# Performance work log

Hardware: AMD Instinct MI355X
Metric: run time of the kernel (lower is better)

The kernel has to match this reference:

```python
import jax, jax.numpy as jnp
import numpy as np

T, H, E, I = 1024, 1024, 64, 512          # tokens, hidden, n_routed_experts, moe_intermediate
NG, TKG, TOPK = 8, 3, 6                   # n_group, topk_group, num_experts_per_tok
NSH = 2                                   # n_shared_experts
RSF = 2.5                                 # routed_scaling_factor
SI = NSH * I                              # shared-expert intermediate


def setup_inputs() -> dict:
    key = jax.random.key(0)
    ks = jax.random.split(key, 9)
    s = 0.02
    return {
        "hidden_states": jax.random.normal(ks[0], (T, H), jnp.float32),
        "gate_w": jax.random.normal(ks[1], (H, E), jnp.float32) * s,
        "e_bias": jax.random.normal(ks[2], (E,), jnp.float32) * s,
        "w_gate": jax.random.normal(ks[3], (E, H, I), jnp.float32) * s,
        "w_up": jax.random.normal(ks[4], (E, H, I), jnp.float32) * s,
        "w_down": jax.random.normal(ks[5], (E, I, H), jnp.float32) * s,
        "sw_gate": jax.random.normal(ks[6], (H, SI), jnp.float32) * s,
        "sw_up": jax.random.normal(ks[7], (H, SI), jnp.float32) * s,
        "sw_down": jax.random.normal(ks[8], (SI, H), jnp.float32) * s,
    }


def _silu_mlp(x, wg, wu, wd):
    # DeepseekV2MLP: down( silu(gate(x)) * up(x) )
    return (jax.nn.silu(x @ wg) * (x @ wu)) @ wd


def _grouped_topk(logits, e_bias):
    # noaux_tc: sigmoid scoring; bias only influences selection, not weights
    scores = jax.nn.sigmoid(logits)                       # [T, E]
    sc = scores + e_bias
    # group score = sum of top-2 biased scores within each group
    gsc = jax.lax.top_k(sc.reshape(-1, NG, E // NG), 2)[0].sum(-1)   # [T, NG]
    gidx = jax.lax.top_k(gsc, TKG)[1]                     # [T, TKG]
    rows = jnp.arange(sc.shape[0])[:, None]
    gmask = jnp.zeros_like(gsc).at[rows, gidx].set(1.0)   # [T, NG]
    emask = jnp.repeat(gmask, E // NG, axis=1) > 0        # [T, E]
    masked = jnp.where(emask, sc, -jnp.inf)
    topk_ids = jax.lax.top_k(masked, TOPK)[1]             # [T, TOPK]
    w = jnp.take_along_axis(scores, topk_ids, axis=1)     # unbiased scores
    w = w / w.sum(-1, keepdims=True)                      # renormalize (norm_topk_prob)
    return w, topk_ids


def reference(hidden_states, gate_w, e_bias, w_gate, w_up, w_down, sw_gate, sw_up, sw_down):
    x = hidden_states
    logits = x @ gate_w                                   # [T, E]
    w, ids = _grouped_topk(logits, e_bias)
    rows = jnp.arange(x.shape[0])[:, None]
    dense_w = jnp.zeros((x.shape[0], E), x.dtype).at[rows, ids].set(w)  # [T, E]

    def body(acc, ws):
        wg, wu, wd, we = ws                               # we: [T] combine weights for this expert
        return acc + we[:, None] * _silu_mlp(x, wg, wu, wd), None

    routed, _ = jax.lax.scan(body, jnp.zeros_like(x), (w_gate, w_up, w_down, dense_w.T))
    shared = _silu_mlp(x, sw_gate, sw_up, sw_down)
    return routed * RSF + shared
```

## Files before the change

kernel.cpp:

```cpp
#include <hip/hip_runtime.h>
#include <hip/hip_bf16.h>

#define T_TOK 1024
#define HDIM  1024
#define NEXP  64
#define IDIM  512
#define SIDIM 1024
#define NGRP  8
#define GSZ   8
#define TKGN  3
#define TOPKN 6
#define CAPS  14336

typedef __attribute__((ext_vector_type(8))) short bf16x8;
typedef __attribute__((ext_vector_type(4))) float f32x4;

__device__ __forceinline__ short f2bf(float f) {
  union { __hip_bfloat16 h; short s; } u;
  u.h = __float2bfloat16(f);
  return u.s;
}
__device__ __forceinline__ float bf2f(short s) {
  union { float f; unsigned u; } c;
  c.u = ((unsigned)(unsigned short)s) << 16;
  return c.f;
}

#define BARRIER() asm volatile("s_waitcnt lgkmcnt(0)\n\ts_barrier" ::: "memory")

__global__ void k0_init(int* counts, int* cursor) {
  int i = threadIdx.x;
  if (i < NEXP) { counts[i] = 0; cursor[i] = 0; }
}

__global__ __launch_bounds__(256) void k1_gate(
    const float* __restrict__ x, const float* __restrict__ gw,
    const float* __restrict__ ebias,
    int* __restrict__ ids, float* __restrict__ wts, int* __restrict__ counts) {
  int sub = threadIdx.x >> 6;
  int lane = threadIdx.x & 63;
  int t = blockIdx.x * 4 + sub;
  const float* xr = x + (size_t)t * HDIM;
  double a0 = 0.0, a1 = 0.0, a2 = 0.0, a3 = 0.0;
  for (int h = 0; h < HDIM; h += 4) {
    float4 xv = *(const float4*)(xr + h);
    a0 += (double)xv.x * (double)gw[(h + 0) * NEXP + lane];
    a1 += (double)xv.y * (double)gw[(h + 1) * NEXP + lane];
    a2 += (double)xv.z * (double)gw[(h + 2) * NEXP + lane];
    a3 += (double)xv.w * (double)gw[(h + 3) * NEXP + lane];
  }
  float logit = (float)((a0 + a1) + (a2 + a3));
  float sig = 1.f / (1.f + expf(-logit));
  float sc = sig + ebias[lane];
  __shared__ float s_sc[4][NEXP], s_sig[4][NEXP];
  s_sc[sub][lane] = sc; s_sig[sub][lane] = sig;
  __syncthreads();
  if (lane == 0) {
    const float* ssc = s_sc[sub];
    const float* ssig = s_sig[sub];
    float gsum[NGRP];
    for (int g = 0; g < NGRP; ++g) {
      float m1 = -1e30f; int i1 = -1;
      for (int i = 0; i < GSZ; ++i) {
        float v = ssc[g * GSZ + i];
        if (v > m1) { m1 = v; i1 = i; }
      }
      float m2 = -1e30f;
      for (int i = 0; i < GSZ; ++i) {
        if (i == i1) continue;
        float v = ssc[g * GSZ + i];
        if (v > m2) m2 = v;
      }
      gsum[g] = m1 + m2;
    }
    unsigned gselmask = 0;
    for (int r = 0; r < TKGN; ++r) {
      float best = -1e30f; int bi = 0;
      for (int g = 0; g < NGRP; ++g) {
        if ((gselmask >> g) & 1) continue;
        if (gsum[g] > best) { best = gsum[g]; bi = g; }
      }
      gselmask |= 1u << bi;
    }
    unsigned long long taken = 0;
    int chosen[TOPKN]; float wsum = 0.f;
    for (int r = 0; r < TOPKN; ++r) {
      float best = -1e30f; int bi = 0;
      for (int e = 0; e < NEXP; ++e) {
        if (!((gselmask >> (e >> 3)) & 1)) continue;
        if ((taken >> e) & 1) continue;
        float v = ssc[e];
        if (v > best) { best = v; bi = e; }
      }
      taken |= 1ull << bi;
      chosen[r] = bi;
      wsum += ssig[bi];
    }
    for (int r = 0; r < TOPKN; ++r) {
      ids[t * TOPKN + r] = chosen[r];
      wts[t * TOPKN + r] = ssig[chosen[r]] / wsum;
      atomicAdd(&counts[chosen[r]], 1);
    }
  }
}

__global__ void k1b_scan(const int* __restrict__ counts, int* __restrict__ eoff,
                         int* __restrict__ tile_e, int* __restrict__ tile_base,
                         int* __restrict__ nt_p, int* __restrict__ slot_tok) {
  __shared__ int soff[NEXP + 1];
  __shared__ int s_total;
  int tid = threadIdx.x;
  if (tid == 0) {
    int o = 0, idx = 0;
    for (int e = 0; e < NEXP; ++e) {
      soff[e] = o;
      int ntile = (counts[e] + 127) >> 7;
      for (int t2 = 0; t2 < ntile; ++t2) { tile_e[idx] = e; tile_base[idx] = o + t2 * 128; ++idx; }
      o += ntile << 7;
    }
    soff[NEXP] = o; nt_p[0] = idx; s_total = o;
  }
  __syncthreads();
  if (tid <= NEXP) eoff[tid] = soff[tid];
  int total = s_total;
  for (int i = tid; i < total; i += blockDim.x) slot_tok[i] = 0;
}

__global__ void k1c_fill(const int* __restrict__ ids,
                         const int* __restrict__ eoff, int* __restrict__ cursor,
                         int* __restrict__ slot_tok, int* __restrict__ tslot) {
  int i = blockIdx.x * blockDim.x + threadIdx.x;
  if (i >= T_TOK * TOPKN) return;
  int e = ids[i];
  int s = eoff[e] + atomicAdd(&cursor[e], 1);
  slot_tok[s] = i / TOPKN;
  tslot[i] = s;
}

__device__ __forceinline__ void tile_mid(
    const float* __restrict__ x, const float* __restrict__ wg, const float* __restrict__ wu,
    const int* __restrict__ slot_tok, int rowbase, int ic0, int IC,
    __hip_bfloat16* __restrict__ mid, short* As, short* Bg, short* Bu) {
  int tid = threadIdx.x;
  int wave = tid >> 6, lane = tid & 63;
  int wm = wave >> 1, wn = wave & 1;
  int lr = lane & 15, lk = lane >> 4;

  int ar = tid >> 3, kg = tid & 7;
  int aw0 = (ar * 8 + (kg ^ (ar & 7))) * 8;
  int aw1 = ((ar + 64) * 8 + (kg ^ (ar & 7))) * 8;
  int tok0 = slot_tok ? slot_tok[rowbase + ar] : (rowbase + ar);
  int tok1 = slot_tok ? slot_tok[rowbase + ar + 64] : (rowbase + ar + 64);
  const float* aptr0 = x + (size_t)tok0 * HDIM + kg * 8;
  const float* aptr1 = x + (size_t)tok1 * HDIM + kg * 8;

  int bn = tid & 63, bkg = tid >> 6;
  const float* bgp = wg + (size_t)(bkg * 8) * IC + ic0 + bn;
  const float* bup = wu + (size_t)(bkg * 8) * IC + ic0 + bn;
  int bw = (bn * 8 + (bkg ^ (bn & 7))) * 8;

  f32x4 accg[2][2], accu[2][2];
  #pragma unroll
  for (int a = 0; a < 2; ++a)
    #pragma unroll
    for (int b = 0; b < 2; ++b) { accg[a][b] = (f32x4)0.f; accu[a][b] = (f32x4)0.f; }

  float4 a00, a01, a10, a11;
  float bgr[8], bur[8];

  auto LOAD = [&](int s) {
    const float* p0 = aptr0 + s * 64;
    const float* p1 = aptr1 + s * 64;
    a00 = *(const float4*)p0; a01 = *(const float4*)(p0 + 4);
    a10 = *(const float4*)p1; a11 = *(const float4*)(p1 + 4);
    #pragma unroll
    for (int i = 0; i < 8; ++i) {
      bgr[i] = bgp[(size_t)(s * 64 + i) * IC];
      bur[i] = bup[(size_t)(s * 64 + i) * IC];
    }
  };
  auto STORE = [&](int b) {
    short* as = As + b * 8192;
    short* bg = Bg + b * 4096;
    short* bu = Bu + b * 4096;
    bf16x8 t0, t1;
    t0[0] = f2bf(a00.x); t0[1] = f2bf(a00.y); t0[2] = f2bf(a00.z); t0[3] = f2bf(a00.w);
    t0[4] = f2bf(a01.x); t0[5] = f2bf(a01.y); t0[6] = f2bf(a01.z); t0[7] = f2bf(a01.w);
    t1[0] = f2bf(a10.x); t1[1] = f2bf(a10.y); t1[2] = f2bf(a10.z); t1[3] = f2bf(a10.w);
    t1[4] = f2bf(a11.x); t1[5] = f2bf(a11.y); t1[6] = f2bf(a11.z); t1[7] = f2bf(a11.w);
    *(bf16x8*)&as[aw0] = t0;
    *(bf16x8*)&as[aw1] = t1;
    bf16x8 tg, tu;
    #pragma unroll
    for (int i = 0; i < 8; ++i) { tg[i] = f2bf(bgr[i]); tu[i] = f2bf(bur[i]); }
    *(bf16x8*)&bg[bw] = tg;
    *(bf16x8*)&bu[bw] = tu;
  };
  auto COMPUTE = [&](int b) {
    const short* as = As + b * 8192;
    const short* bg = Bg + b * 4096;
    const short* bu = Bu + b * 4096;
    #pragma unroll
    for (int kk = 0; kk < 2; ++kk) {
      bf16x8 af[2];
      #pragma unroll
      for (int mf = 0; mf < 2; ++mf) {
        int row = wm * 32 + mf * 16 + lr;
        af[mf] = *(const bf16x8*)&as[(row * 8 + ((kk * 4 + lk) ^ (row & 7))) * 8];
      }
      #pragma unroll
      for (int nf = 0; nf < 2; ++nf) {
        int col = wn * 32 + nf * 16 + lr;
        int gi = (col * 8 + ((kk * 4 + lk) ^ (col & 7))) * 8;
        bf16x8 bgf = *(const bf16x8*)&bg[gi];
        bf16x8 buf_ = *(const bf16x8*)&bu[gi];
        #pragma unroll
        for (int mf = 0; mf < 2; ++mf) {
          accg[mf][nf] = __builtin_amdgcn_mfma_f32_16x16x32_bf16(af[mf], bgf, accg[mf][nf], 0, 0, 0);
          accu[mf][nf] = __builtin_amdgcn_mfma_f32_16x16x32_bf16(af[mf], buf_, accu[mf][nf], 0, 0, 0);
        }
      }
    }
  };

  const int NST = HDIM / 64;
  LOAD(0);
  STORE(0);
  LOAD(1);
  BARRIER();
  for (int s = 0; s < NST; ++s) {
    COMPUTE(s & 1);
    if (s + 1 < NST) {
      STORE((s + 1) & 1);
      if (s + 2 < NST) LOAD(s + 2);
      BARRIER();
    }
  }

  #pragma unroll
  for (int mf = 0; mf < 2; ++mf)
    #pragma unroll
    for (int nf = 0; nf < 2; ++nf)
      #pragma unroll
      for (int r = 0; r < 4; ++r) {
        int row = wm * 32 + mf * 16 + lk * 4 + r;
        int col = wn * 32 + nf * 16 + lr;
        float gv = accg[mf][nf][r], uv = accu[mf][nf][r];
        float h = gv / (1.f + expf(-gv)) * uv;
        mid[(size_t)(rowbase + row) * IC + ic0 + col] = __float2bfloat16(h);
      }
}

__device__ __forceinline__ void tile_down(
    const __hip_bfloat16* __restrict__ mid, const float* __restrict__ wd,
    int rowbase, int n0, int KD,
    __hip_bfloat16* __restrict__ dout, short* As, short* Bs) {
  int tid = threadIdx.x;
  int wave = tid >> 6, lane = tid & 63;
  int wm = wave >> 1, wn = wave & 1;
  int lr = lane & 15, lk = lane >> 4;

  int ar = tid >> 3, kg = tid & 7;
  int aw0 = (ar * 8 + (kg ^ (ar & 7))) * 8;
  int aw1 = ((ar + 64) * 8 + (kg ^ (ar & 7))) * 8;
  const __hip_bfloat16* aptr0 = mid + (size_t)(rowbase + ar) * KD + kg * 8;
  const __hip_bfloat16* aptr1 = mid + (size_t)(rowbase + ar + 64) * KD + kg * 8;

  int bn = tid & 63, bkg = tid >> 6;
  const float* bp = wd + (size_t)(bkg * 8) * HDIM + n0 + bn;
  int bw = (bn * 8 + (bkg ^ (bn & 7))) * 8;

  f32x4 acc[2][2];
  #pragma unroll
  for (int a = 0; a < 2; ++a)
    #pragma unroll
    for (int b = 0; b < 2; ++b) acc[a][b] = (f32x4)0.f;

  bf16x8 av0, av1;
  float br[8];

  auto LOAD = [&](int s) {
    av0 = *(const bf16x8*)(aptr0 + s * 64);
    av1 = *(const bf16x8*)(aptr1 + s * 64);
    #pragma unroll
    for (int i = 0; i < 8; ++i) br[i] = bp[(size_t)(s * 64 + i) * HDIM];
  };
  auto STORE = [&](int b) {
    short* as = As + b * 8192;
    short* bs = Bs + b * 4096;
    *(bf16x8*)&as[aw0] = av0;
    *(bf16x8*)&as[aw1] = av1;
    bf16x8 tb;
    #pragma unroll
    for (int i = 0; i < 8; ++i) tb[i] = f2bf(br[i]);
    *(bf16x8*)&bs[bw] = tb;
  };
  auto COMPUTE = [&](int b) {
    const short* as = As + b * 8192;
    const short* bs = Bs + b * 4096;
    #pragma unroll
    for (int kk = 0; kk < 2; ++kk) {
      bf16x8 af[2];
      #pragma unroll
      for (int mf = 0; mf < 2; ++mf) {
        int row = wm * 32 + mf * 16 + lr;
        af[mf] = *(const bf16x8*)&as[(row * 8 + ((kk * 4 + lk) ^ (row & 7))) * 8];
      }
      #pragma unroll
      for (int nf = 0; nf < 2; ++nf) {
        int col = wn * 32 + nf * 16 + lr;
        bf16x8 bf_ = *(const bf16x8*)&bs[(col * 8 + ((kk * 4 + lk) ^ (col & 7))) * 8];
        #pragma unroll
        for (int mf = 0; mf < 2; ++mf)
          acc[mf][nf] = __builtin_amdgcn_mfma_f32_16x16x32_bf16(af[mf], bf_, acc[mf][nf], 0, 0, 0);
      }
    }
  };

  const int NST = KD / 64;
  LOAD(0);
  STORE(0);
  LOAD(1);
  BARRIER();
  for (int s = 0; s < NST; ++s) {
    COMPUTE(s & 1);
    if (s + 1 < NST) {
      STORE((s + 1) & 1);
      if (s + 2 < NST) LOAD(s + 2);
      BARRIER();
    }
  }

  #pragma unroll
  for (int mf = 0; mf < 2; ++mf)
    #pragma unroll
    for (int nf = 0; nf < 2; ++nf)
      #pragma unroll
      for (int r = 0; r < 4; ++r) {
        int row = wm * 32 + mf * 16 + lk * 4 + r;
        int col = wn * 32 + nf * 16 + lr;
        dout[(size_t)(rowbase + row) * HDIM + n0 + col] = __float2bfloat16(acc[mf][nf][r]);
      }
}

__global__ __launch_bounds__(512) void k2_fused(
    const float* __restrict__ x, const float* __restrict__ Wg, const float* __restrict__ Wu,
    const float* __restrict__ swg, const float* __restrict__ swu,
    const int* __restrict__ slot_tok, const int* __restrict__ tile_e,
    const int* __restrict__ tile_base, const int* __restrict__ nt_p,
    __hip_bfloat16* __restrict__ mid_r, __hip_bfloat16* __restrict__ mid_s) {
  __shared__ __align__(16) short As[2 * 8192];
  __shared__ __align__(16) short Bg[2 * 4096];
  __shared__ __align__(16) short Bu[2 * 4096];
  int nrt = nt_p[0] * 8;
  int nitems = nrt + 128;
  for (int item = blockIdx.x; item < nitems; item += gridDim.x) {
    if (item < nrt) {
      int tile = item >> 3, c = item & 7;
      int e = tile_e[tile];
      tile_mid(x, Wg + (size_t)e * HDIM * IDIM, Wu + (size_t)e * HDIM * IDIM,
               slot_tok, tile_base[tile], c * 64, IDIM, mid_r, As, Bg, Bu);
    } else {
      int it = item - nrt;
      int mt = it >> 4, c = it & 15;
      tile_mid(x, swg, swu, nullptr, mt * 128, c * 64, SIDIM, mid_s, As, Bg, Bu);
    }
  }
}

__global__ __launch_bounds__(512) void k3_fused(
    const __hip_bfloat16* __restrict__ mid_r, const __hip_bfloat16* __restrict__ mid_s,
    const float* __restrict__ Wd, const float* __restrict__ swd,
    const int* __restrict__ tile_e, const int* __restrict__ tile_base,
    const int* __restrict__ nt_p,
    __hip_bfloat16* __restrict__ dout_r, __hip_bfloat16* __restrict__ dout_s) {
  __shared__ __align__(16) short As[2 * 8192];
  __shared__ __align__(16) short Bs[2 * 4096];
  int nrt = nt_p[0] * 16;
  int nsh = 128;
  int nitems = nrt + nsh;
  for (int item = blockIdx.x; item < nitems; item += gridDim.x) {
    if (item < nsh) {
      int mt = item >> 4, c = item & 15;
      tile_down(mid_s, swd, mt * 128, c * 64, SIDIM, dout_s, As, Bs);
    } else {
      int it = item - nsh;
      int tile = it >> 4, c = it & 15;
      int e = tile_e[tile];
      tile_down(mid_r, Wd + (size_t)e * IDIM * HDIM, tile_base[tile], c * 64, IDIM,
                dout_r, As, Bs);
    }
  }
}

__global__ __launch_bounds__(128) void k4_combine(
    const __hip_bfloat16* __restrict__ dout_r, const __hip_bfloat16* __restrict__ dout_s,
    const int* __restrict__ tslot, const float* __restrict__ wts,
    float* __restrict__ out) {
  int t = blockIdx.x;
  int tid = threadIdx.x;
  int sl[TOPKN]; float w[TOPKN];
  #pragma unroll
  for (int r = 0; r < TOPKN; ++r) {
    sl[r] = tslot[t * TOPKN + r];
    w[r] = wts[t * TOPKN + r] * 2.5f;
  }
  int h0 = tid * 8;
  float acc[8];
  bf16x8 vs = *(const bf16x8*)((const short*)dout_s + (size_t)t * HDIM + h0);
  #pragma unroll
  for (int j = 0; j < 8; ++j) acc[j] = bf2f(vs[j]);
  #pragma unroll
  for (int r = 0; r < TOPKN; ++r) {
    bf16x8 v = *(const bf16x8*)((const short*)dout_r + (size_t)sl[r] * HDIM + h0);
    #pragma unroll
    for (int j = 0; j < 8; ++j) acc[j] += w[r] * bf2f(v[j]);
  }
  float* op = out + (size_t)t * HDIM + h0;
  float4 o0 = make_float4(acc[0], acc[1], acc[2], acc[3]);
  float4 o1 = make_float4(acc[4], acc[5], acc[6], acc[7]);
  *(float4*)op = o0;
  *(float4*)(op + 4) = o1;
}

extern "C" void kernel_launch(void* const* d_in, const int* in_sizes, int n_in,
                              void* d_out, int out_size, void* d_ws, size_t ws_size,
                              hipStream_t stream) {
  (void)in_sizes; (void)n_in; (void)out_size; (void)ws_size;
  const float* x      = (const float*)d_in[0];
  const float* gate_w = (const float*)d_in[1];
  const float* ebias  = (const float*)d_in[2];
  const float* wgate  = (const float*)d_in[3];
  const float* wup    = (const float*)d_in[4];
  const float* wdown  = (const float*)d_in[5];
  const float* swg    = (const float*)d_in[6];
  const float* swu    = (const float*)d_in[7];
  const float* swd    = (const float*)d_in[8];
  float* out = (float*)d_out;

  char* ws = (char*)d_ws;
  int*   counts    = (int*)(ws + 0);
  int*   cursor    = (int*)(ws + 256);
  int*   eoff      = (int*)(ws + 512);
  int*   nt_p      = (int*)(ws + 1024);
  int*   tile_e    = (int*)(ws + 1088);
  int*   tile_base = (int*)(ws + 1600);
  int*   ids       = (int*)(ws + 4096);
  float* wts       = (float*)(ws + 28672);
  int*   tslot     = (int*)(ws + 53248);
  int*   slot_tok  = (int*)(ws + 77824);
  __hip_bfloat16* mid_r  = (__hip_bfloat16*)(ws + 135168);
  __hip_bfloat16* mid_s  = mid_r + (size_t)CAPS * IDIM;
  __hip_bfloat16* dout_r = (__hip_bfloat16*)(ws + 16912384);
  __hip_bfloat16* dout_s = dout_r + (size_t)CAPS * HDIM;

  k0_init<<<1, 128, 0, stream>>>(counts, cursor);
  k1_gate<<<T_TOK / 4, 256, 0, stream>>>(x, gate_w, ebias, ids, wts, counts);
  k1b_scan<<<1, 256, 0, stream>>>(counts, eoff, tile_e, tile_base, nt_p, slot_tok);
  k1c_fill<<<(T_TOK * TOPKN + 255) / 256, 256, 0, stream>>>(ids, eoff, cursor, slot_tok, tslot);
  k2_fused<<<640, 512, 0, stream>>>(x, wgate, wup, swg, swu, slot_tok, tile_e, tile_base, nt_p, mid_r, mid_s);
  k3_fused<<<1152, 512, 0, stream>>>(mid_r, mid_s, wdown, swd, tile_e, tile_base, nt_p, dout_r, dout_s);
  k4_combine<<<T_TOK, 128, 0, stream>>>(dout_r, dout_s, tslot, wts, out);
}
```

Measured before the change: 232.5 us.

## Deepen weight prefetch to two stages ahead and cap occupancy in MoE GEMM kernels

Splits the A and B tile loads and keeps two register sets of weight values, so fp32 weight loads are issued two K-steps ahead instead of one, and unrolls the main loop by two with fixed LDS buffers. It also adds a min-blocks-per-SM hint of 4 to both fused GEMM kernels and changes the persistent grid sizes to 512 blocks. The aim is to hide global-memory latency on the strided weight reads. The cost is extra registers under a tighter register budget, which could cause spills.

```diff
diff --git a/kernel.cpp b/kernel.cpp
--- a/kernel.cpp
+++ b/kernel.cpp
@@ -166,20 +166,22 @@
     for (int b = 0; b < 2; ++b) { accg[a][b] = (f32x4)0.f; accu[a][b] = (f32x4)0.f; }
 
   float4 a00, a01, a10, a11;
-  float bgr[8], bur[8];
-
-  auto LOAD = [&](int s) {
+  float g0[8], u0[8], g1[8], u1[8];
+
+  auto LOADA = [&](int s) {
     const float* p0 = aptr0 + s * 64;
     const float* p1 = aptr1 + s * 64;
     a00 = *(const float4*)p0; a01 = *(const float4*)(p0 + 4);
     a10 = *(const float4*)p1; a11 = *(const float4*)(p1 + 4);
+  };
+  auto LOADB = [&](float (&g)[8], float (&u)[8], int s) {
     #pragma unroll
     for (int i = 0; i < 8; ++i) {
-      bgr[i] = bgp[(size_t)(s * 64 + i) * IC];
-      bur[i] = bup[(size_t)(s * 64 + i) * IC];
-    }
-  };
-  auto STORE = [&](int b) {
+      g[i] = bgp[(size_t)(s * 64 + i) * IC];
+      u[i] = bup[(size_t)(s * 64 + i) * IC];
+    }
+  };
+  auto STORE = [&](int b, float (&g)[8], float (&u)[8]) {
     short* as = As + b * 8192;
     short* bg = Bg + b * 4096;
     short* bu = Bu + b * 4096;
@@ -192,7 +194,7 @@
     *(bf16x8*)&as[aw1] = t1;
     bf16x8 tg, tu;
     #pragma unroll
-    for (int i = 0; i < 8; ++i) { tg[i] = f2bf(bgr[i]); tu[i] = f2bf(bur[i]); }
+    for (int i = 0; i < 8; ++i) { tg[i] = f2bf(g[i]); tu[i] = f2bf(u[i]); }
     *(bf16x8*)&bg[bw] = tg;
     *(bf16x8*)&bu[bw] = tu;
   };
@@ -224,15 +226,24 @@
   };
 
   const int NST = HDIM / 64;
-  LOAD(0);
-  STORE(0);
-  LOAD(1);
+  LOADB(g0, u0, 0);
+  LOADB(g1, u1, 1);
+  LOADA(0);
+  STORE(0, g0, u0);
+  LOADA(1);
+  LOADB(g0, u0, 2);
   BARRIER();
-  for (int s = 0; s < NST; ++s) {
-    COMPUTE(s & 1);
-    if (s + 1 < NST) {
-      STORE((s + 1) & 1);
-      if (s + 2 < NST) LOAD(s + 2);
+  for (int s = 0; s < NST; s += 2) {
+    COMPUTE(0);
+    STORE(1, g1, u1);
+    if (s + 2 < NST) LOADA(s + 2);
+    if (s + 3 < NST) LOADB(g1, u1, s + 3);
+    BARRIER();
+    COMPUTE(1);
+    if (s + 2 < NST) {
+      STORE(0, g0, u0);
+      if (s + 3 < NST) LOADA(s + 3);
+      if (s + 4 < NST) LOADB(g0, u0, s + 4);
       BARRIER();
     }
   }
@@ -277,27 +288,29 @@
     for (int b = 0; b < 2; ++b) acc[a][b] = (f32x4)0.f;
 
   bf16x8 av0, av1;
-  float br[8];
-
-  auto LOAD = [&](int s) {
+  float b0[8], b1[8];
+
+  auto LOADA = [&](int s) {
     av0 = *(const bf16x8*)(aptr0 + s * 64);
     av1 = *(const bf16x8*)(aptr1 + s * 64);
-    #pragma unroll
-    for (int i = 0; i < 8; ++i) br[i] = bp[(size_t)(s * 64 + i) * HDIM];
-  };
-  auto STORE = [&](int b) {
-    short* as = As + b * 8192;
-    short* bs = Bs + b * 4096;
+  };
+  auto LOADB = [&](float (&b)[8], int s) {
+    #pragma unroll
+    for (int i = 0; i < 8; ++i) b[i] = bp[(size_t)(s * 64 + i) * HDIM];
+  };
+  auto STORE = [&](int bb, float (&b)[8]) {
+    short* as = As + bb * 8192;
+    short* bs = Bs + bb * 4096;
     *(bf16x8*)&as[aw0] = av0;
     *(bf16x8*)&as[aw1] = av1;
     bf16x8 tb;
     #pragma unroll
-    for (int i = 0; i < 8; ++i) tb[i] = f2bf(br[i]);
+    for (int i = 0; i < 8; ++i) tb[i] = f2bf(b[i]);
     *(bf16x8*)&bs[bw] = tb;
   };
-  auto COMPUTE = [&](int b) {
-    const short* as = As + b * 8192;
-    const short* bs = Bs + b * 4096;
+  auto COMPUTE = [&](int bb) {
+    const short* as = As + bb * 8192;
+    const short* bs = Bs + bb * 4096;
     #pragma unroll
     for (int kk = 0; kk < 2; ++kk) {
       bf16x8 af[2];
@@ -318,15 +331,24 @@
   };
 
   const int NST = KD / 64;
-  LOAD(0);
-  STORE(0);
-  LOAD(1);
+  LOADB(b0, 0);
+  LOADB(b1, 1);
+  LOADA(0);
+  STORE(0, b0);
+  LOADA(1);
+  LOADB(b0, 2);
   BARRIER();
-  for (int s = 0; s < NST; ++s) {
-    COMPUTE(s & 1);
-    if (s + 1 < NST) {
-      STORE((s + 1) & 1);
-      if (s + 2 < NST) LOAD(s + 2);
+  for (int s = 0; s < NST; s += 2) {
+    COMPUTE(0);
+    STORE(1, b1);
+    if (s + 2 < NST) LOADA(s + 2);
+    if (s + 3 < NST) LOADB(b1, s + 3);
+    BARRIER();
+    COMPUTE(1);
+    if (s + 2 < NST) {
+      STORE(0, b0);
+      if (s + 3 < NST) LOADA(s + 3);
+      if (s + 4 < NST) LOADB(b0, s + 4);
       BARRIER();
     }
   }
@@ -343,7 +365,7 @@
       }
 }
 
-__global__ __launch_bounds__(512) void k2_fused(
+__global__ __launch_bounds__(512, 4) void k2_fused(
     const float* __restrict__ x, const float* __restrict__ Wg, const float* __restrict__ Wu,
     const float* __restrict__ swg, const float* __restrict__ swu,
     const int* __restrict__ slot_tok, const int* __restrict__ tile_e,
@@ -368,7 +390,7 @@
   }
 }
 
-__global__ __launch_bounds__(512) void k3_fused(
+__global__ __launch_bounds__(512, 4) void k3_fused(
     const __hip_bfloat16* __restrict__ mid_r, const __hip_bfloat16* __restrict__ mid_s,
     const float* __restrict__ Wd, const float* __restrict__ swd,
     const int* __restrict__ tile_e, const int* __restrict__ tile_base,
@@ -458,7 +480,7 @@
   k1_gate<<<T_TOK / 4, 256, 0, stream>>>(x, gate_w, ebias, ids, wts, counts);
   k1b_scan<<<1, 256, 0, stream>>>(counts, eoff, tile_e, tile_base, nt_p, slot_tok);
   k1c_fill<<<(T_TOK * TOPKN + 255) / 256, 256, 0, stream>>>(ids, eoff, cursor, slot_tok, tslot);
-  k2_fused<<<640, 512, 0, stream>>>(x, wgate, wup, swg, swu, slot_tok, tile_e, tile_base, nt_p, mid_r, mid_s);
-  k3_fused<<<1152, 512, 0, stream>>>(mid_r, mid_s, wdown, swd, tile_e, tile_base, nt_p, dout_r, dout_s);
+  k2_fused<<<512, 512, 0, stream>>>(x, wgate, wup, swg, swu, slot_tok, tile_e, tile_base, nt_p, mid_r, mid_s);
+  k3_fused<<<512, 512, 0, stream>>>(mid_r, mid_s, wdown, swd, tile_e, tile_base, nt_p, dout_r, dout_s);
   k4_combine<<<T_TOK, 128, 0, stream>>>(dout_r, dout_s, tslot, wts, out);
 }
```

Result: slower. 246.8 us (+6.2%).

## Pre-transpose weights to bf16 and stage GEMM tiles via direct global-to-LDS loads

Applied to the files above, without the earlier changes.

Adds kernels that convert x to bf16 and transpose every expert and shared weight into K-contiguous bf16 layouts each call. The GEMM tiles then stage A and B with global_load_lds 16-byte copies into swizzled LDS, replacing strided fp32 scalar loads and register conversion. The persistent grid loops become one tile per block with an XCD-aware block remap. The cost is an extra full read and write of all weights (about 200MB of fp32 input) every call, plus more kernel launches.

```diff
diff --git a/kernel.cpp b/kernel.cpp
--- a/kernel.cpp
+++ b/kernel.cpp
@@ -26,11 +26,57 @@
   return c.f;
 }
 
-#define BARRIER() asm volatile("s_waitcnt lgkmcnt(0)\n\ts_barrier" ::: "memory")
+__device__ __forceinline__ void gld16(const void* g, void* l) {
+  typedef __attribute__((address_space(1))) const unsigned int GU;
+  typedef __attribute__((address_space(3))) unsigned int LU;
+  __builtin_amdgcn_global_load_lds((GU*)g, (LU*)l, 16, 0, 0);
+}
+
+#define PIPE_BARRIER() asm volatile("s_waitcnt vmcnt(0) lgkmcnt(0)\n\ts_barrier" ::: "memory")
 
 __global__ void k0_init(int* counts, int* cursor) {
   int i = threadIdx.x;
   if (i < NEXP) { counts[i] = 0; cursor[i] = 0; }
+}
+
+__global__ __launch_bounds__(128) void kx_conv(const float* __restrict__ x,
+                                               __hip_bfloat16* __restrict__ xb) {
+  int row = blockIdx.x;
+  int c = threadIdx.x * 8;
+  const float* s = x + (size_t)row * HDIM + c;
+  float4 v0 = *(const float4*)s;
+  float4 v1 = *(const float4*)(s + 4);
+  bf16x8 o;
+  o[0] = f2bf(v0.x); o[1] = f2bf(v0.y); o[2] = f2bf(v0.z); o[3] = f2bf(v0.w);
+  o[4] = f2bf(v1.x); o[5] = f2bf(v1.y); o[6] = f2bf(v1.z); o[7] = f2bf(v1.w);
+  *(bf16x8*)((short*)xb + (size_t)row * HDIM + c) = o;
+}
+
+__global__ __launch_bounds__(256) void kt_transpose(
+    const float* __restrict__ src, __hip_bfloat16* __restrict__ dst, int R, int C) {
+  __shared__ float t[64 * 65];
+  int m = blockIdx.z;
+  const float* s = src + (size_t)m * R * C + (size_t)(blockIdx.x * 64) * C + blockIdx.y * 64;
+  short* d = (short*)dst + (size_t)m * R * C + (size_t)(blockIdx.y * 64) * R + blockIdx.x * 64;
+  int tid = threadIdx.x;
+  int r = tid >> 2, c16 = (tid & 3) * 16;
+  const float* sp = s + (size_t)r * C + c16;
+  #pragma unroll
+  for (int j = 0; j < 4; ++j) {
+    float4 v = *(const float4*)(sp + j * 4);
+    t[r * 65 + c16 + j * 4 + 0] = v.x;
+    t[r * 65 + c16 + j * 4 + 1] = v.y;
+    t[r * 65 + c16 + j * 4 + 2] = v.z;
+    t[r * 65 + c16 + j * 4 + 3] = v.w;
+  }
+  __syncthreads();
+  bf16x8 o0, o1;
+  #pragma unroll
+  for (int j = 0; j < 8; ++j) o0[j] = f2bf(t[(c16 + j) * 65 + r]);
+  #pragma unroll
+  for (int j = 0; j < 8; ++j) o1[j] = f2bf(t[(c16 + 8 + j) * 65 + r]);
+  *(bf16x8*)(d + (size_t)r * R + c16) = o0;
+  *(bf16x8*)(d + (size_t)r * R + c16 + 8) = o1;
 }
 
 __global__ __launch_bounds__(256) void k1_gate(
@@ -137,27 +183,26 @@
   tslot[i] = s;
 }
 
-__device__ __forceinline__ void tile_mid(
-    const float* __restrict__ x, const float* __restrict__ wg, const float* __restrict__ wu,
+__device__ __forceinline__ void tile_mid2(
+    const __hip_bfloat16* __restrict__ xb,
+    const __hip_bfloat16* __restrict__ wtg, const __hip_bfloat16* __restrict__ wtu,
     const int* __restrict__ slot_tok, int rowbase, int ic0, int IC,
-    __hip_bfloat16* __restrict__ mid, short* As, short* Bg, short* Bu) {
+    __hip_bfloat16* __restrict__ mid,
+    short* As, short* Bg, short* Bu) {
   int tid = threadIdx.x;
   int wave = tid >> 6, lane = tid & 63;
   int wm = wave >> 1, wn = wave & 1;
   int lr = lane & 15, lk = lane >> 4;
 
-  int ar = tid >> 3, kg = tid & 7;
-  int aw0 = (ar * 8 + (kg ^ (ar & 7))) * 8;
-  int aw1 = ((ar + 64) * 8 + (kg ^ (ar & 7))) * 8;
-  int tok0 = slot_tok ? slot_tok[rowbase + ar] : (rowbase + ar);
-  int tok1 = slot_tok ? slot_tok[rowbase + ar + 64] : (rowbase + ar + 64);
-  const float* aptr0 = x + (size_t)tok0 * HDIM + kg * 8;
-  const float* aptr1 = x + (size_t)tok1 * HDIM + kg * 8;
-
-  int bn = tid & 63, bkg = tid >> 6;
-  const float* bgp = wg + (size_t)(bkg * 8) * IC + ic0 + bn;
-  const float* bup = wu + (size_t)(bkg * 8) * IC + ic0 + bn;
-  int bw = (bn * 8 + (bkg ^ (bn & 7))) * 8;
+  int srow = wave * 8 + (lane >> 3);
+  int kgl = (lane & 7) ^ (srow & 7);
+  int t0 = slot_tok ? slot_tok[rowbase + srow] : (rowbase + srow);
+  int t1 = slot_tok ? slot_tok[rowbase + srow + 64] : (rowbase + srow + 64);
+  const short* ga0 = (const short*)xb + (size_t)t0 * HDIM + kgl * 8;
+  const short* ga1 = (const short*)xb + (size_t)t1 * HDIM + kgl * 8;
+  const short* gbg = (const short*)wtg + (size_t)(ic0 + srow) * HDIM + kgl * 8;
+  const short* gbu = (const short*)wtu + (size_t)(ic0 + srow) * HDIM + kgl * 8;
+  int ldsoff = wave * 1024;
 
   f32x4 accg[2][2], accu[2][2];
   #pragma unroll
@@ -165,53 +210,31 @@
     #pragma unroll
     for (int b = 0; b < 2; ++b) { accg[a][b] = (f32x4)0.f; accu[a][b] = (f32x4)0.f; }
 
-  float4 a00, a01, a10, a11;
-  float bgr[8], bur[8];
-
-  auto LOAD = [&](int s) {
-    const float* p0 = aptr0 + s * 64;
-    const float* p1 = aptr1 + s * 64;
-    a00 = *(const float4*)p0; a01 = *(const float4*)(p0 + 4);
-    a10 = *(const float4*)p1; a11 = *(const float4*)(p1 + 4);
-    #pragma unroll
-    for (int i = 0; i < 8; ++i) {
-      bgr[i] = bgp[(size_t)(s * 64 + i) * IC];
-      bur[i] = bup[(size_t)(s * 64 + i) * IC];
-    }
+  auto STAGE = [&](int buf, int s) {
+    char* a = (char*)As + buf * 16384 + ldsoff;
+    char* bg = (char*)Bg + buf * 8192 + ldsoff;
+    char* bu = (char*)Bu + buf * 8192 + ldsoff;
+    gld16(ga0 + s * 64, a);
+    gld16(ga1 + s * 64, a + 8192);
+    gld16(gbg + s * 64, bg);
+    gld16(gbu + s * 64, bu);
   };
-  auto STORE = [&](int b) {
-    short* as = As + b * 8192;
-    short* bg = Bg + b * 4096;
-    short* bu = Bu + b * 4096;
-    bf16x8 t0, t1;
-    t0[0] = f2bf(a00.x); t0[1] = f2bf(a00.y); t0[2] = f2bf(a00.z); t0[3] = f2bf(a00.w);
-    t0[4] = f2bf(a01.x); t0[5] = f2bf(a01.y); t0[6] = f2bf(a01.z); t0[7] = f2bf(a01.w);
-    t1[0] = f2bf(a10.x); t1[1] = f2bf(a10.y); t1[2] = f2bf(a10.z); t1[3] = f2bf(a10.w);
-    t1[4] = f2bf(a11.x); t1[5] = f2bf(a11.y); t1[6] = f2bf(a11.z); t1[7] = f2bf(a11.w);
-    *(bf16x8*)&as[aw0] = t0;
-    *(bf16x8*)&as[aw1] = t1;
-    bf16x8 tg, tu;
-    #pragma unroll
-    for (int i = 0; i < 8; ++i) { tg[i] = f2bf(bgr[i]); tu[i] = f2bf(bur[i]); }
-    *(bf16x8*)&bg[bw] = tg;
-    *(bf16x8*)&bu[bw] = tu;
-  };
-  auto COMPUTE = [&](int b) {
-    const short* as = As + b * 8192;
-    const short* bg = Bg + b * 4096;
-    const short* bu = Bu + b * 4096;
+  auto COMPUTE = [&](int buf) {
+    const short* as = As + buf * 8192;
+    const short* bg = Bg + buf * 4096;
+    const short* bu = Bu + buf * 4096;
     #pragma unroll
     for (int kk = 0; kk < 2; ++kk) {
       bf16x8 af[2];
       #pragma unroll
       for (int mf = 0; mf < 2; ++mf) {
         int row = wm * 32 + mf * 16 + lr;
-        af[mf] = *(const bf16x8*)&as[(row * 8 + ((kk * 4 + lk) ^ (row & 7))) * 8];
+        af[mf] = *(const bf16x8*)&as[row * 64 + (((kk * 4 + lk) ^ (row & 7)) * 8)];
       }
       #pragma unroll
       for (int nf = 0; nf < 2; ++nf) {
         int col = wn * 32 + nf * 16 + lr;
-        int gi = (col * 8 + ((kk * 4 + lk) ^ (col & 7))) * 8;
+        int gi = col * 64 + (((kk * 4 + lk) ^ (col & 7)) * 8);
         bf16x8 bgf = *(const bf16x8*)&bg[gi];
         bf16x8 buf_ = *(const bf16x8*)&bu[gi];
         #pragma unroll
@@ -224,17 +247,12 @@
   };
 
   const int NST = HDIM / 64;
-  LOAD(0);
-  STORE(0);
-  LOAD(1);
-  BARRIER();
+  STAGE(0, 0);
+  PIPE_BARRIER();
   for (int s = 0; s < NST; ++s) {
+    if (s + 1 < NST) STAGE((s + 1) & 1, s + 1);
     COMPUTE(s & 1);
-    if (s + 1 < NST) {
-      STORE((s + 1) & 1);
-      if (s + 2 < NST) LOAD(s + 2);
-      BARRIER();
-    }
+    PIPE_BARRIER();
   }
 
   #pragma unroll
@@ -251,8 +269,8 @@
       }
 }
 
-__device__ __forceinline__ void tile_down(
-    const __hip_bfloat16* __restrict__ mid, const float* __restrict__ wd,
+__device__ __forceinline__ void tile_down2(
+    const __hip_bfloat16* __restrict__ mid, const __hip_bfloat16* __restrict__ wtd,
     int rowbase, int n0, int KD,
     __hip_bfloat16* __restrict__ dout, short* As, short* Bs) {
   int tid = threadIdx.x;
@@ -260,15 +278,12 @@
   int wm = wave >> 1, wn = wave & 1;
   int lr = lane & 15, lk = lane >> 4;
 
-  int ar = tid >> 3, kg = tid & 7;
-  int aw0 = (ar * 8 + (kg ^ (ar & 7))) * 8;
-  int aw1 = ((ar + 64) * 8 + (kg ^ (ar & 7))) * 8;
-  const __hip_bfloat16* aptr0 = mid + (size_t)(rowbase + ar) * KD + kg * 8;
-  const __hip_bfloat16* aptr1 = mid + (size_t)(rowbase + ar + 64) * KD + kg * 8;
-
-  int bn = tid & 63, bkg = tid >> 6;
-  const float* bp = wd + (size_t)(bkg * 8) * HDIM + n0 + bn;
-  int bw = (bn * 8 + (bkg ^ (bn & 7))) * 8;
+  int srow = wave * 8 + (lane >> 3);
+  int kgl = (lane & 7) ^ (srow & 7);
+  const short* ga0 = (const short*)mid + (size_t)(rowbase + srow) * KD + kgl * 8;
+  const short* ga1 = (const short*)mid + (size_t)(rowbase + srow + 64) * KD + kgl * 8;
+  const short* gb = (const short*)wtd + (size_t)(n0 + srow) * KD + kgl * 8;
+  int ldsoff = wave * 1024;
 
   f32x4 acc[2][2];
   #pragma unroll
@@ -276,40 +291,28 @@
     #pragma unroll
     for (int b = 0; b < 2; ++b) acc[a][b] = (f32x4)0.f;
 
-  bf16x8 av0, av1;
-  float br[8];
-
-  auto LOAD = [&](int s) {
-    av0 = *(const bf16x8*)(aptr0 + s * 64);
-    av1 = *(const bf16x8*)(aptr1 + s * 64);
-    #pragma unroll
-    for (int i = 0; i < 8; ++i) br[i] = bp[(size_t)(s * 64 + i) * HDIM];
+  auto STAGE = [&](int buf, int s) {
+    char* a = (char*)As + buf * 16384 + ldsoff;
+    char* bs = (char*)Bs + buf * 8192 + ldsoff;
+    gld16(ga0 + s * 64, a);
+    gld16(ga1 + s * 64, a + 8192);
+    gld16(gb + s * 64, bs);
   };
-  auto STORE = [&](int b) {
-    short* as = As + b * 8192;
-    short* bs = Bs + b * 4096;
-    *(bf16x8*)&as[aw0] = av0;
-    *(bf16x8*)&as[aw1] = av1;
-    bf16x8 tb;
-    #pragma unroll
-    for (int i = 0; i < 8; ++i) tb[i] = f2bf(br[i]);
-    *(bf16x8*)&bs[bw] = tb;
-  };
-  auto COMPUTE = [&](int b) {
-    const short* as = As + b * 8192;
-    const short* bs = Bs + b * 4096;
+  auto COMPUTE = [&](int buf) {
+    const short* as = As + buf * 8192;
+    const short* bs = Bs + buf * 4096;
     #pragma unroll
     for (int kk = 0; kk < 2; ++kk) {
       bf16x8 af[2];
       #pragma unroll
       for (int mf = 0; mf < 2; ++mf) {
         int row = wm * 32 + mf * 16 + lr;
-        af[mf] = *(const bf16x8*)&as[(row * 8 + ((kk * 4 + lk) ^ (row & 7))) * 8];
+        af[mf] = *(const bf16x8*)&as[row * 64 + (((kk * 4 + lk) ^ (row & 7)) * 8)];
       }
       #pragma unroll
       for (int nf = 0; nf < 2; ++nf) {
         int col = wn * 32 + nf * 16 + lr;
-        bf16x8 bf_ = *(const bf16x8*)&bs[(col * 8 + ((kk * 4 + lk) ^ (col & 7))) * 8];
+        bf16x8 bf_ = *(const bf16x8*)&bs[col * 64 + (((kk * 4 + lk) ^ (col & 7)) * 8)];
         #pragma unroll
         for (int mf = 0; mf < 2; ++mf)
           acc[mf][nf] = __builtin_amdgcn_mfma_f32_16x16x32_bf16(af[mf], bf_, acc[mf][nf], 0, 0, 0);
@@ -318,17 +321,12 @@
   };
 
   const int NST = KD / 64;
-  LOAD(0);
-  STORE(0);
-  LOAD(1);
-  BARRIER();
+  STAGE(0, 0);
+  PIPE_BARRIER();
   for (int s = 0; s < NST; ++s) {
+    if (s + 1 < NST) STAGE((s + 1) & 1, s + 1);
     COMPUTE(s & 1);
-    if (s + 1 < NST) {
-      STORE((s + 1) & 1);
-      if (s + 2 < NST) LOAD(s + 2);
-      BARRIER();
-    }
+    PIPE_BARRIER();
   }
 
   #pragma unroll
@@ -344,52 +342,54 @@
 }
 
 __global__ __launch_bounds__(512) void k2_fused(
-    const float* __restrict__ x, const float* __restrict__ Wg, const float* __restrict__ Wu,
-    const float* __restrict__ swg, const float* __restrict__ swu,
+    const __hip_bfloat16* __restrict__ xb,
+    const __hip_bfloat16* __restrict__ wt_g, const __hip_bfloat16* __restrict__ wt_u,
+    const __hip_bfloat16* __restrict__ ts_g, const __hip_bfloat16* __restrict__ ts_u,
     const int* __restrict__ slot_tok, const int* __restrict__ tile_e,
     const int* __restrict__ tile_base, const int* __restrict__ nt_p,
     __hip_bfloat16* __restrict__ mid_r, __hip_bfloat16* __restrict__ mid_s) {
   __shared__ __align__(16) short As[2 * 8192];
   __shared__ __align__(16) short Bg[2 * 4096];
   __shared__ __align__(16) short Bu[2 * 4096];
+  int q = gridDim.x >> 3;
+  int item = (blockIdx.x & 7) * q + (blockIdx.x >> 3);
   int nrt = nt_p[0] * 8;
   int nitems = nrt + 128;
-  for (int item = blockIdx.x; item < nitems; item += gridDim.x) {
-    if (item < nrt) {
-      int tile = item >> 3, c = item & 7;
-      int e = tile_e[tile];
-      tile_mid(x, Wg + (size_t)e * HDIM * IDIM, Wu + (size_t)e * HDIM * IDIM,
-               slot_tok, tile_base[tile], c * 64, IDIM, mid_r, As, Bg, Bu);
-    } else {
-      int it = item - nrt;
-      int mt = it >> 4, c = it & 15;
-      tile_mid(x, swg, swu, nullptr, mt * 128, c * 64, SIDIM, mid_s, As, Bg, Bu);
-    }
+  if (item >= nitems) return;
+  if (item < nrt) {
+    int tile = item >> 3, c = item & 7;
+    int e = tile_e[tile];
+    tile_mid2(xb, wt_g + (size_t)e * IDIM * HDIM, wt_u + (size_t)e * IDIM * HDIM,
+              slot_tok, tile_base[tile], c * 64, IDIM, mid_r, As, Bg, Bu);
+  } else {
+    int it = item - nrt;
+    int mt = it >> 4, c = it & 15;
+    tile_mid2(xb, ts_g, ts_u, nullptr, mt * 128, c * 64, SIDIM, mid_s, As, Bg, Bu);
   }
 }
 
 __global__ __launch_bounds__(512) void k3_fused(
     const __hip_bfloat16* __restrict__ mid_r, const __hip_bfloat16* __restrict__ mid_s,
-    const float* __restrict__ Wd, const float* __restrict__ swd,
+    const __hip_bfloat16* __restrict__ wt_d, const __hip_bfloat16* __restrict__ ts_d,
     const int* __restrict__ tile_e, const int* __restrict__ tile_base,
     const int* __restrict__ nt_p,
     __hip_bfloat16* __restrict__ dout_r, __hip_bfloat16* __restrict__ dout_s) {
   __shared__ __align__(16) short As[2 * 8192];
   __shared__ __align__(16) short Bs[2 * 4096];
-  int nrt = nt_p[0] * 16;
+  int q = gridDim.x >> 3;
+  int item = (blockIdx.x & 7) * q + (blockIdx.x >> 3);
   int nsh = 128;
-  int nitems = nrt + nsh;
-  for (int item = blockIdx.x; item < nitems; item += gridDim.x) {
-    if (item < nsh) {
-      int mt = item >> 4, c = item & 15;
-      tile_down(mid_s, swd, mt * 128, c * 64, SIDIM, dout_s, As, Bs);
-    } else {
-      int it = item - nsh;
-      int tile = it >> 4, c = it & 15;
-      int e = tile_e[tile];
-      tile_down(mid_r, Wd + (size_t)e * IDIM * HDIM, tile_base[tile], c * 64, IDIM,
-                dout_r, As, Bs);
-    }
+  int nitems = nsh + nt_p[0] * 16;
+  if (item >= nitems) return;
+  if (item < nsh) {
+    int mt = item >> 4, c = item & 15;
+    tile_down2(mid_s, ts_d, mt * 128, c * 64, SIDIM, dout_s, As, Bs);
+  } else {
+    int it = item - nsh;
+    int tile = it >> 4, c = it & 15;
+    int e = tile_e[tile];
+    tile_down2(mid_r, wt_d + (size_t)e * HDIM * IDIM, tile_base[tile], c * 64, IDIM,
+               dout_r, As, Bs);
   }
 }
 
@@ -417,10 +417,8 @@
     for (int j = 0; j < 8; ++j) acc[j] += w[r] * bf2f(v[j]);
   }
   float* op = out + (size_t)t * HDIM + h0;
-  float4 o0 = make_float4(acc[0], acc[1], acc[2], acc[3]);
-  float4 o1 = make_float4(acc[4], acc[5], acc[6], acc[7]);
-  *(float4*)op = o0;
-  *(float4*)(op + 4) = o1;
+  *(float4*)op = make_float4(acc[0], acc[1], acc[2], acc[3]);
+  *(float4*)(op + 4) = make_float4(acc[4], acc[5], acc[6], acc[7]);
 }
 
 extern "C" void kernel_launch(void* const* d_in, const int* in_sizes, int n_in,
@@ -444,21 +442,37 @@
   int*   eoff      = (int*)(ws + 512);
   int*   nt_p      = (int*)(ws + 1024);
   int*   tile_e    = (int*)(ws + 1088);
-  int*   tile_base = (int*)(ws + 1600);
+  int*   tile_base = (int*)(ws + 2112);
   int*   ids       = (int*)(ws + 4096);
   float* wts       = (float*)(ws + 28672);
   int*   tslot     = (int*)(ws + 53248);
   int*   slot_tok  = (int*)(ws + 77824);
-  __hip_bfloat16* mid_r  = (__hip_bfloat16*)(ws + 135168);
-  __hip_bfloat16* mid_s  = mid_r + (size_t)CAPS * IDIM;
-  __hip_bfloat16* dout_r = (__hip_bfloat16*)(ws + 16912384);
-  __hip_bfloat16* dout_s = dout_r + (size_t)CAPS * HDIM;
+  __hip_bfloat16* xb   = (__hip_bfloat16*)(ws + 262144);
+  __hip_bfloat16* wt_g = (__hip_bfloat16*)(ws + 4194304);
+  __hip_bfloat16* wt_u = (__hip_bfloat16*)(ws + 71303168);
+  __hip_bfloat16* ts_g = (__hip_bfloat16*)(ws + 138412032);
+  __hip_bfloat16* ts_u = (__hip_bfloat16*)(ws + 140509184);
+  __hip_bfloat16* wt_d = (__hip_bfloat16*)(ws + 4194304);
+  __hip_bfloat16* ts_d = (__hip_bfloat16*)(ws + 71303168);
+  __hip_bfloat16* dout_r = (__hip_bfloat16*)(ws + 73400320);
+  __hip_bfloat16* dout_s = (__hip_bfloat16*)(ws + 102760448);
+  __hip_bfloat16* mid_r = (__hip_bfloat16*)(ws + 142606336);
+  __hip_bfloat16* mid_s = (__hip_bfloat16*)(ws + 157286400);
 
   k0_init<<<1, 128, 0, stream>>>(counts, cursor);
+  kx_conv<<<T_TOK, 128, 0, stream>>>(x, xb);
+  kt_transpose<<<dim3(16, 8, NEXP), 256, 0, stream>>>(wgate, wt_g, HDIM, IDIM);
+  kt_transpose<<<dim3(16, 8, NEXP), 256, 0, stream>>>(wup, wt_u, HDIM, IDIM);
+  kt_transpose<<<dim3(16, 16, 1), 256, 0, stream>>>(swg, ts_g, HDIM, SIDIM);
+  kt_transpose<<<dim3(16, 16, 1), 256, 0, stream>>>(swu, ts_u, HDIM, SIDIM);
   k1_gate<<<T_TOK / 4, 256, 0, stream>>>(x, gate_w, ebias, ids, wts, counts);
   k1b_scan<<<1, 256, 0, stream>>>(counts, eoff, tile_e, tile_base, nt_p, slot_tok);
   k1c_fill<<<(T_TOK * TOPKN + 255) / 256, 256, 0, stream>>>(ids, eoff, cursor, slot_tok, tslot);
-  k2_fused<<<640, 512, 0, stream>>>(x, wgate, wup, swg, swu, slot_tok, tile_e, tile_base, nt_p, mid_r, mid_s);
-  k3_fused<<<1152, 512, 0, stream>>>(mid_r, mid_s, wdown, swd, tile_e, tile_base, nt_p, dout_r, dout_s);
+  k2_fused<<<1024, 512, 0, stream>>>(xb, wt_g, wt_u, ts_g, ts_u, slot_tok,
+                                     tile_e, tile_base, nt_p, mid_r, mid_s);
+  kt_transpose<<<dim3(8, 16, NEXP), 256, 0, stream>>>(wdown, wt_d, IDIM, HDIM);
+  kt_transpose<<<dim3(16, 16, 1), 256, 0, stream>>>(swd, ts_d, SIDIM, HDIM);
+  k3_fused<<<1920, 512, 0, stream>>>(mid_r, mid_s, wt_d, ts_d, tile_e, tile_base,
+                                     nt_p, dout_r, dout_s);
   k4_combine<<<T_TOK, 128, 0, stream>>>(dout_r, dout_s, tslot, wts, out);
 }
```

Result: slower. 369.8 us (+59.0%).
